# Optimization experiments

Hardware: AMD Instinct MI355X
Metric: run time of the kernel (lower is better)

The kernel has to match this reference:

```python
import jax, jax.numpy as jnp
import numpy as np

N, E = 50000, 800000
IN_DIM, HID, HEADS, OUT_DIM, NUM_CLASSES = 512, 128, 4, 64, 4


def setup_inputs() -> dict:
    key = jax.random.key(0)
    ks = jax.random.split(key, 18)
    g = lambda k, shape, s=0.05: (jax.random.normal(k, shape, dtype=jnp.float32) * s)
    x = jax.random.normal(ks[0], (N, IN_DIM), dtype=jnp.float32)
    edge_index = jax.random.randint(ks[1], (2, E), 0, N, dtype=jnp.int32)
    return {
        "x": x,
        "edge_index": edge_index,
        # GATConv layer 1 (heads=4, concat)
        "W1": g(ks[2], (IN_DIM, HEADS * HID)),
        "att_src1": g(ks[3], (HEADS, HID)),
        "att_dst1": g(ks[4], (HEADS, HID)),
        "b1": jnp.zeros((HEADS * HID,), jnp.float32),
        # GATConv layer 2 (heads=1, no concat)
        "W2": g(ks[5], (HEADS * HID, OUT_DIM)),
        "att_src2": g(ks[6], (1, OUT_DIM)),
        "att_dst2": g(ks[7], (1, OUT_DIM)),
        "b2": jnp.zeros((OUT_DIM,), jnp.float32),
        # intra_attention MLP: Linear(out,out) -> tanh -> Linear(out,1) -> softmax(dim=0)
        "Wa": g(ks[8], (OUT_DIM, OUT_DIM)),
        "ba": jnp.zeros((OUT_DIM,), jnp.float32),
        "wv": g(ks[9], (OUT_DIM, 1)),
        "bv": jnp.zeros((1,), jnp.float32),
        "class_attn": g(ks[10], (NUM_CLASSES, OUT_DIM), 0.3),
        # classifier
        "Wc": g(ks[11], (OUT_DIM, NUM_CLASSES)),
        "bc": jnp.zeros((NUM_CLASSES,), jnp.float32),
    }


def _gat_layer(x, src, dst, W, att_src, att_dst, heads, feat):
    """PyG GATConv: gather -> LeakyReLU score -> segment softmax -> scatter add."""
    n = x.shape[0]
    h = (x @ W).reshape(n, heads, feat)                     # [N,H,F]
    a_s = jnp.sum(h * att_src[None], axis=-1)               # [N,H]
    a_d = jnp.sum(h * att_dst[None], axis=-1)               # [N,H]
    e = jax.nn.leaky_relu(a_s[src] + a_d[dst], 0.2)         # [E,H]
    m = jax.ops.segment_max(e, dst, num_segments=n)         # per-dst max
    ex = jnp.exp(e - m[dst])
    s = jax.ops.segment_sum(ex, dst, num_segments=n)
    alpha = ex / (s[dst] + 1e-16)                           # [E,H]
    msg = h[src] * alpha[:, :, None]                        # [E,H,F]
    return jax.ops.segment_sum(msg, dst, num_segments=n)    # [N,H,F]


def reference(x, edge_index, W1, att_src1, att_dst1, b1, W2, att_src2, att_dst2,
              b2, Wa, ba, wv, bv, class_attn, Wc, bc):
    n = x.shape[0]
    loop = jnp.arange(n, dtype=edge_index.dtype)
    src = jnp.concatenate([edge_index[0], loop])            # add_self_loops=True
    dst = jnp.concatenate([edge_index[1], loop])

    h1 = _gat_layer(x, src, dst, W1, att_src1, att_dst1, HEADS, HID)
    h1 = h1.reshape(n, HEADS * HID) + b1                    # concat heads + bias
    h1 = jax.nn.elu(h1)

    h2 = _gat_layer(h1, src, dst, W2, att_src2, att_dst2, 1, OUT_DIM)
    h2 = h2.reshape(n, OUT_DIM) + b2                        # heads=1, concat=False

    # intra-sample attention, softmax over nodes (dim=0)
    scores = jnp.tanh(h2 @ Wa + ba) @ wv + bv               # [N,1]
    attw = jax.nn.softmax(scores, axis=0)
    xw = h2 * attw                                          # [N,OUT]

    xn = xw / jnp.maximum(jnp.linalg.norm(xw, axis=1, keepdims=True), 1e-12)
    cn = class_attn / jnp.maximum(
        jnp.linalg.norm(class_attn, axis=1, keepdims=True), 1e-12)
    inter_class_scores = xn @ cn.T                          # [N,C]

    out = xw @ Wc + bc                                      # [N,C]
    return out, xw, inter_class_scores
```

## Files before the change

### kernel.cpp

```cpp
#include <hip/hip_runtime.h>
#include <cstdint>
#include <cstddef>

typedef __attribute__((ext_vector_type(8))) short bf16x8;
typedef __attribute__((ext_vector_type(4))) float f32x4;
typedef __attribute__((ext_vector_type(8))) unsigned short u16x8;

__device__ __forceinline__ unsigned encf(float f) {
  unsigned u = __float_as_uint(f);
  return (u & 0x80000000u) ? ~u : (u | 0x80000000u);
}
__device__ __forceinline__ float decf(unsigned u) {
  return (u & 0x80000000u) ? __uint_as_float(u & 0x7FFFFFFFu) : __uint_as_float(~u);
}
__device__ __forceinline__ float lrelu02(float x) { return x > 0.f ? x : 0.2f * x; }
__device__ __forceinline__ unsigned short f2bf(float f) {
  unsigned u = __float_as_uint(f);
  unsigned r = u + 0x7FFFu + ((u >> 16) & 1u);
  return (unsigned short)(r >> 16);
}
__device__ __forceinline__ float bf2f(unsigned short b) {
  return __uint_as_float(((unsigned)b) << 16);
}

__device__ __forceinline__ void gll16(const void* g, void* l) {
  __builtin_amdgcn_global_load_lds(
      (const __attribute__((address_space(1))) void*)g,
      (__attribute__((address_space(3))) void*)l, 16, 0, 0);
}

__global__ void zero_int_k(int* __restrict__ p, int n) {
  int i = blockIdx.x * 256 + threadIdx.x;
  if (i < n) p[i] = 0;
}

__global__ void hist_k(const int* __restrict__ ei, int E, int N, int* __restrict__ counts) {
  int i = blockIdx.x * 256 + threadIdx.x;
  int Eall = E + N;
  if (i >= Eall) return;
  int dst = (i < E) ? ei[E + i] : (i - E);
  atomicAdd(&counts[dst], 1);
}

__global__ __launch_bounds__(256) void scan1_k(const int* __restrict__ counts,
                                               int* __restrict__ incl,
                                               int* __restrict__ bsum, int N) {
  int b = blockIdx.x, tid = threadIdx.x;
  int lane = tid & 63, wv = tid >> 6;
  int i = b * 256 + tid;
  int v = (i < N) ? counts[i] : 0;
#pragma unroll
  for (int o = 1; o < 64; o <<= 1) {
    int t = __shfl_up(v, o, 64);
    if (lane >= o) v += t;
  }
  __shared__ int wsum[4];
  if (lane == 63) wsum[wv] = v;
  __syncthreads();
  int base = 0;
  for (int wj = 0; wj < wv; wj++) base += wsum[wj];
  v += base;
  if (i < N) incl[i] = v;
  if (tid == 255) bsum[b] = v;
}

__global__ __launch_bounds__(256) void scan2_k(const int* __restrict__ bsum,
                                               int* __restrict__ pb, int nb) {
  int tid = threadIdx.x;
  int lane = tid & 63, wv = tid >> 6;
  int v = (tid < nb) ? bsum[tid] : 0;
  int orig = v;
#pragma unroll
  for (int o = 1; o < 64; o <<= 1) {
    int t = __shfl_up(v, o, 64);
    if (lane >= o) v += t;
  }
  __shared__ int wsum[4];
  if (lane == 63) wsum[wv] = v;
  __syncthreads();
  int base = 0;
  for (int wj = 0; wj < wv; wj++) base += wsum[wj];
  if (tid < nb) pb[tid] = v + base - orig;
}

__global__ void scan3_k(const int* __restrict__ incl, const int* __restrict__ pb,
                        int* __restrict__ offs, int* __restrict__ cursor, int N) {
  int i = blockIdx.x * 256 + threadIdx.x;
  if (i == 0) { offs[0] = 0; cursor[0] = 0; }
  if (i < N) {
    int v = incl[i] + pb[i >> 8];
    offs[i + 1] = v;
    if (i + 1 < N) cursor[i + 1] = v;
  }
}

__global__ void scatter_k(const int* __restrict__ ei, int E, int N,
                          int* __restrict__ cursor, int* __restrict__ ssrc) {
  int i = blockIdx.x * 256 + threadIdx.x;
  int Eall = E + N;
  if (i >= Eall) return;
  int src, dst;
  if (i < E) { src = ei[i]; dst = ei[E + i]; }
  else       { src = i - E; dst = i - E; }
  int pos = atomicAdd(&cursor[dst], 1);
  ssrc[pos] = src;
}

__global__ void conv_x_k(const float* __restrict__ x, unsigned short* __restrict__ xb,
                         int N, int Mpad) {
  int i = blockIdx.x * 256 + threadIdx.x;
  int total = Mpad * 64;
  if (i >= total) return;
  int row = i >> 6;
  u16x8 v;
  if (row < N) {
    const float4* src = (const float4*)(x + (size_t)i * 8);
    float4 a = src[0], b = src[1];
    v[0] = f2bf(a.x); v[1] = f2bf(a.y); v[2] = f2bf(a.z); v[3] = f2bf(a.w);
    v[4] = f2bf(b.x); v[5] = f2bf(b.y); v[6] = f2bf(b.z); v[7] = f2bf(b.w);
  } else {
    v = (u16x8)0;
  }
  *(u16x8*)(xb + (size_t)i * 8) = v;
}

__global__ void conv_wt_k(const float* __restrict__ W, unsigned short* __restrict__ Wt,
                          int K, int Nc) {
  int i = blockIdx.x * 256 + threadIdx.x;
  if (i >= K * Nc) return;
  int c = i / K, k = i - c * K;
  Wt[i] = f2bf(W[(size_t)k * Nc + c]);
}

__global__ __launch_bounds__(256, 2) void gemm1_k(const unsigned short* __restrict__ A,
                                                  const unsigned short* __restrict__ Bt,
                                                  unsigned short* __restrict__ C,
                                                  const float* __restrict__ att_s,
                                                  const float* __restrict__ att_d,
                                                  float* __restrict__ as_out,
                                                  float* __restrict__ ad_out,
                                                  int M, int K, int Nc) {
  __shared__ unsigned short As[128][64];
  __shared__ unsigned short Bs[256][64];
  __shared__ float s_ds[2][128];
  __shared__ float s_dd[2][128];
  const int tid = threadIdx.x;
  const int lane = tid & 63;
  const int w = tid >> 6;
  const int wr = w >> 1, wc = w & 1;
  const int l16 = lane & 15, lk = lane >> 4;
  const int row0 = blockIdx.x * 128, col0 = blockIdx.y * 256;

  f32x4 acc[4][8];
#pragma unroll
  for (int m = 0; m < 4; m++)
#pragma unroll
    for (int n = 0; n < 8; n++) acc[m][n] = (f32x4)0.f;

  const char* Abase = (const char*)A;
  const char* Bbase = (const char*)Bt;

  for (int k0 = 0; k0 < K; k0 += 64) {
#pragma unroll
    for (int i = 0; i < 4; i++) {
      int ca = i * 256 + tid;
      int r = ca >> 3, b = (ca & 7) * 16;
      gll16(Abase + ((size_t)(row0 + r) * K + k0) * 2 + b, (char*)&As[0][0] + ca * 16);
    }
#pragma unroll
    for (int i = 0; i < 8; i++) {
      int cb = i * 256 + tid;
      int c = cb >> 3, b = (cb & 7) * 16;
      gll16(Bbase + ((size_t)(col0 + c) * K + k0) * 2 + b, (char*)&Bs[0][0] + cb * 16);
    }
    __syncthreads();
#pragma unroll
    for (int ks = 0; ks < 2; ks++) {
      bf16x8 af[4], bfr[8];
#pragma unroll
      for (int m = 0; m < 4; m++)
        af[m] = *(const bf16x8*)&As[wr * 64 + m * 16 + l16][ks * 32 + lk * 8];
#pragma unroll
      for (int n = 0; n < 8; n++)
        bfr[n] = *(const bf16x8*)&Bs[wc * 128 + n * 16 + l16][ks * 32 + lk * 8];
#pragma unroll
      for (int m = 0; m < 4; m++)
#pragma unroll
        for (int n = 0; n < 8; n++)
          acc[m][n] = __builtin_amdgcn_mfma_f32_16x16x32_bf16(af[m], bfr[n], acc[m][n], 0, 0, 0);
    }
    __syncthreads();
  }
#pragma unroll
  for (int m = 0; m < 4; m++) {
    int row_b = row0 + wr * 64 + m * 16 + lk * 4;
#pragma unroll
    for (int r = 0; r < 4; r++) {
      int row = row_b + r;
      if (row < M) {
#pragma unroll
        for (int n = 0; n < 8; n++) {
          int col = col0 + wc * 128 + n * 16 + l16;
          C[(size_t)row * Nc + col] = f2bf(acc[m][n][r]);
        }
      }
    }
  }
  float as_c[8], ad_c[8];
#pragma unroll
  for (int n = 0; n < 8; n++) {
    int col = col0 + wc * 128 + n * 16 + l16;
    as_c[n] = att_s[col];
    ad_c[n] = att_d[col];
  }
#pragma unroll
  for (int m = 0; m < 4; m++) {
#pragma unroll
    for (int r = 0; r < 4; r++) {
      float ps = 0.f, pd = 0.f;
#pragma unroll
      for (int n = 0; n < 8; n++) {
        ps += acc[m][n][r] * as_c[n];
        pd += acc[m][n][r] * ad_c[n];
      }
#pragma unroll
      for (int o = 8; o; o >>= 1) { ps += __shfl_xor(ps, o); pd += __shfl_xor(pd, o); }
      if (l16 == 0) {
        int rr = wr * 64 + m * 16 + lk * 4 + r;
        s_ds[wc][rr] = ps;
        s_dd[wc][rr] = pd;
      }
    }
  }
  __syncthreads();
  if (tid < 128) {
    int row = row0 + tid;
    if (row < M) {
      int hb = 2 * blockIdx.y;
      as_out[(size_t)row * 4 + hb + 0] = s_ds[0][tid];
      as_out[(size_t)row * 4 + hb + 1] = s_ds[1][tid];
      ad_out[(size_t)row * 4 + hb + 0] = s_dd[0][tid];
      ad_out[(size_t)row * 4 + hb + 1] = s_dd[1][tid];
    }
  }
}

__global__ __launch_bounds__(256) void gemm2_k(const unsigned short* __restrict__ A,
                                               const unsigned short* __restrict__ Bt,
                                               unsigned short* __restrict__ C,
                                               const float* __restrict__ att_s,
                                               const float* __restrict__ att_d,
                                               float* __restrict__ as_out,
                                               float* __restrict__ ad_out,
                                               int M, int K, int Nc) {
  __shared__ unsigned short As[64][64];
  __shared__ unsigned short Bs[64][64];
  __shared__ float s_ds[2][64];
  __shared__ float s_dd[2][64];
  const int tid = threadIdx.x;
  const int lane = tid & 63;
  const int w = tid >> 6;
  const int wr = w >> 1, wc = w & 1;
  const int l16 = lane & 15, lk = lane >> 4;
  const int row0 = blockIdx.x * 64;

  f32x4 acc[2][2];
#pragma unroll
  for (int m = 0; m < 2; m++)
#pragma unroll
    for (int n = 0; n < 2; n++) acc[m][n] = (f32x4)0.f;

  const char* Abase = (const char*)A;
  const char* Bbase = (const char*)Bt;

  for (int k0 = 0; k0 < K; k0 += 64) {
#pragma unroll
    for (int i = 0; i < 2; i++) {
      int ca = i * 256 + tid;
      int r = ca >> 3, b = (ca & 7) * 16;
      gll16(Abase + ((size_t)(row0 + r) * K + k0) * 2 + b, (char*)&As[0][0] + ca * 16);
    }
#pragma unroll
    for (int i = 0; i < 2; i++) {
      int cb = i * 256 + tid;
      int c = cb >> 3, b = (cb & 7) * 16;
      gll16(Bbase + ((size_t)c * K + k0) * 2 + b, (char*)&Bs[0][0] + cb * 16);
    }
    __syncthreads();
#pragma unroll
    for (int ks = 0; ks < 2; ks++) {
      bf16x8 af[2], bfr[2];
#pragma unroll
      for (int m = 0; m < 2; m++)
        af[m] = *(const bf16x8*)&As[wr * 32 + m * 16 + l16][ks * 32 + lk * 8];
#pragma unroll
      for (int n = 0; n < 2; n++)
        bfr[n] = *(const bf16x8*)&Bs[wc * 32 + n * 16 + l16][ks * 32 + lk * 8];
#pragma unroll
      for (int m = 0; m < 2; m++)
#pragma unroll
        for (int n = 0; n < 2; n++)
          acc[m][n] = __builtin_amdgcn_mfma_f32_16x16x32_bf16(af[m], bfr[n], acc[m][n], 0, 0, 0);
    }
    __syncthreads();
  }
#pragma unroll
  for (int m = 0; m < 2; m++) {
    int row_b = row0 + wr * 32 + m * 16 + lk * 4;
#pragma unroll
    for (int r = 0; r < 4; r++) {
      int row = row_b + r;
      if (row < M) {
#pragma unroll
        for (int n = 0; n < 2; n++) {
          int col = wc * 32 + n * 16 + l16;
          C[(size_t)row * Nc + col] = f2bf(acc[m][n][r]);
        }
      }
    }
  }
  float as_c[2], ad_c[2];
#pragma unroll
  for (int n = 0; n < 2; n++) {
    int col = wc * 32 + n * 16 + l16;
    as_c[n] = att_s[col];
    ad_c[n] = att_d[col];
  }
#pragma unroll
  for (int m = 0; m < 2; m++) {
#pragma unroll
    for (int r = 0; r < 4; r++) {
      float ps = 0.f, pd = 0.f;
#pragma unroll
      for (int n = 0; n < 2; n++) {
        ps += acc[m][n][r] * as_c[n];
        pd += acc[m][n][r] * ad_c[n];
      }
#pragma unroll
      for (int o = 8; o; o >>= 1) { ps += __shfl_xor(ps, o); pd += __shfl_xor(pd, o); }
      if (l16 == 0) {
        int rr = wr * 32 + m * 16 + lk * 4 + r;
        s_ds[wc][rr] = ps;
        s_dd[wc][rr] = pd;
      }
    }
  }
  __syncthreads();
  if (tid < 64) {
    int row = row0 + tid;
    if (row < M) {
      as_out[row] = s_ds[0][tid] + s_ds[1][tid];
      ad_out[row] = s_dd[0][tid] + s_dd[1][tid];
    }
  }
}

__global__ __launch_bounds__(256) void gat_agg1_k(const unsigned short* __restrict__ hfeat,
                                                  const float* __restrict__ a_s,
                                                  const float* __restrict__ a_d,
                                                  const int* __restrict__ offs,
                                                  const int* __restrict__ ssrc,
                                                  const float* __restrict__ b1,
                                                  unsigned short* __restrict__ h1b, int N) {
  const int tid = threadIdx.x;
  const int lane = tid & 63, wave = tid >> 6;
  const int n = blockIdx.x * 4 + wave;
  if (n >= N) return;
  __shared__ int   s_src[4][64];
  __shared__ float s_ex[4][64][4];
  const int start = offs[n], end = offs[n + 1];
  const int hhl = lane >> 4;
  const float4 adv4 = *(const float4*)(a_d + (size_t)n * 4);
  const float4* as4 = (const float4*)a_s;

  float m0 = -1e30f, m1 = -1e30f, m2 = -1e30f, m3 = -1e30f;
  float S0 = 0.f, S1 = 0.f, S2 = 0.f, S3 = 0.f;
  float acc[8] = {0.f, 0.f, 0.f, 0.f, 0.f, 0.f, 0.f, 0.f};

  for (int base = start; base < end; base += 64) {
    const int cnt = min(64, end - base);
    float e0 = -1e30f, e1 = -1e30f, e2 = -1e30f, e3 = -1e30f;
    int s = 0;
    if (lane < cnt) {
      s = ssrc[base + lane];
      float4 av = as4[s];
      e0 = lrelu02(av.x + adv4.x);
      e1 = lrelu02(av.y + adv4.y);
      e2 = lrelu02(av.z + adv4.z);
      e3 = lrelu02(av.w + adv4.w);
    }
    float c0 = e0, c1 = e1, c2 = e2, c3 = e3;
#pragma unroll
    for (int o = 32; o; o >>= 1) {
      c0 = fmaxf(c0, __shfl_xor(c0, o));
      c1 = fmaxf(c1, __shfl_xor(c1, o));
      c2 = fmaxf(c2, __shfl_xor(c2, o));
      c3 = fmaxf(c3, __shfl_xor(c3, o));
    }
    float nm0 = fmaxf(m0, c0), nm1 = fmaxf(m1, c1);
    float nm2 = fmaxf(m2, c2), nm3 = fmaxf(m3, c3);
    float sc0 = __expf(m0 - nm0), sc1 = __expf(m1 - nm1);
    float sc2 = __expf(m2 - nm2), sc3 = __expf(m3 - nm3);
    m0 = nm0; m1 = nm1; m2 = nm2; m3 = nm3;
    float x0 = (lane < cnt) ? __expf(e0 - nm0) : 0.f;
    float x1 = (lane < cnt) ? __expf(e1 - nm1) : 0.f;
    float x2 = (lane < cnt) ? __expf(e2 - nm2) : 0.f;
    float x3 = (lane < cnt) ? __expf(e3 - nm3) : 0.f;
    s_src[wave][lane] = s;
    s_ex[wave][lane][0] = x0; s_ex[wave][lane][1] = x1;
    s_ex[wave][lane][2] = x2; s_ex[wave][lane][3] = x3;
#pragma unroll
    for (int o = 32; o; o >>= 1) {
      x0 += __shfl_xor(x0, o); x1 += __shfl_xor(x1, o);
      x2 += __shfl_xor(x2, o); x3 += __shfl_xor(x3, o);
    }
    S0 = S0 * sc0 + x0; S1 = S1 * sc1 + x1;
    S2 = S2 * sc2 + x2; S3 = S3 * sc3 + x3;
    float scl = (hhl == 0) ? sc0 : (hhl == 1) ? sc1 : (hhl == 2) ? sc2 : sc3;
#pragma unroll
    for (int q = 0; q < 8; q++) acc[q] *= scl;
#pragma unroll 4
    for (int j = 0; j < cnt; j++) {
      int sj = s_src[wave][j];
      float al = s_ex[wave][j][hhl];
      uint4 pk = *(const uint4*)(hfeat + ((size_t)sj << 9) + lane * 8);
      acc[0] += al * __uint_as_float(pk.x << 16);
      acc[1] += al * __uint_as_float(pk.x & 0xFFFF0000u);
      acc[2] += al * __uint_as_float(pk.y << 16);
      acc[3] += al * __uint_as_float(pk.y & 0xFFFF0000u);
      acc[4] += al * __uint_as_float(pk.z << 16);
      acc[5] += al * __uint_as_float(pk.z & 0xFFFF0000u);
      acc[6] += al * __uint_as_float(pk.w << 16);
      acc[7] += al * __uint_as_float(pk.w & 0xFFFF0000u);
    }
  }
  float inv = 1.f / (((hhl == 0) ? S0 : (hhl == 1) ? S1 : (hhl == 2) ? S2 : S3) + 1e-16f);
  const float4 b1a = *(const float4*)(b1 + lane * 8);
  const float4 b1b = *(const float4*)(b1 + lane * 8 + 4);
  float v[8];
  v[0] = acc[0] * inv + b1a.x; v[1] = acc[1] * inv + b1a.y;
  v[2] = acc[2] * inv + b1a.z; v[3] = acc[3] * inv + b1a.w;
  v[4] = acc[4] * inv + b1b.x; v[5] = acc[5] * inv + b1b.y;
  v[6] = acc[6] * inv + b1b.z; v[7] = acc[7] * inv + b1b.w;
  u16x8 outv;
#pragma unroll
  for (int q = 0; q < 8; q++) {
    float t = v[q] > 0.f ? v[q] : (__expf(v[q]) - 1.f);
    outv[q] = f2bf(t);
  }
  *(u16x8*)(h1b + ((size_t)n << 9) + lane * 8) = outv;
}

__global__ __launch_bounds__(256) void gat_agg2_k(const unsigned short* __restrict__ h2b,
                                                  const float* __restrict__ a_s,
                                                  const float* __restrict__ a_d,
                                                  const int* __restrict__ offs,
                                                  const int* __restrict__ ssrc,
                                                  const float* __restrict__ b2,
                                                  float* __restrict__ h2out, int N) {
  const int tid = threadIdx.x;
  const int lane = tid & 63, wave = tid >> 6;
  const int n = blockIdx.x * 4 + wave;
  if (n >= N) return;
  __shared__ int   s_src[4][64];
  __shared__ float s_ex[4][64];
  const int start = offs[n], end = offs[n + 1];
  const float ad = a_d[n];
  const int half = lane >> 5, l32 = lane & 31;

  float m = -1e30f, S = 0.f, acc0 = 0.f, acc1 = 0.f;
  for (int base = start; base < end; base += 64) {
    const int cnt = min(64, end - base);
    float e = -1e30f;
    int s = 0;
    if (lane < cnt) {
      s = ssrc[base + lane];
      e = lrelu02(a_s[s] + ad);
    }
    float c = e;
#pragma unroll
    for (int o = 32; o; o >>= 1) c = fmaxf(c, __shfl_xor(c, o));
    float nm = fmaxf(m, c);
    float sc = __expf(m - nm);
    m = nm;
    float x = (lane < cnt) ? __expf(e - nm) : 0.f;
    s_src[wave][lane] = s;
    s_ex[wave][lane] = x;
    float xs = x;
#pragma unroll
    for (int o = 32; o; o >>= 1) xs += __shfl_xor(xs, o);
    S = S * sc + xs;
    acc0 *= sc; acc1 *= sc;
#pragma unroll 4
    for (int j = half; j < cnt; j += 2) {
      int sj = s_src[wave][j];
      float al = s_ex[wave][j];
      unsigned pk = *(const unsigned*)(h2b + ((size_t)sj << 6) + l32 * 2);
      acc0 += al * __uint_as_float(pk << 16);
      acc1 += al * __uint_as_float(pk & 0xFFFF0000u);
    }
  }
  acc0 += __shfl_xor(acc0, 32);
  acc1 += __shfl_xor(acc1, 32);
  if (half == 0) {
    float inv = 1.f / (S + 1e-16f);
    float2 o;
    o.x = acc0 * inv + b2[l32 * 2];
    o.y = acc1 * inv + b2[l32 * 2 + 1];
    *(float2*)(h2out + ((size_t)n << 6) + l32 * 2) = o;
  }
}

__global__ __launch_bounds__(256) void score_k(const float* __restrict__ h2,
                                               const float* __restrict__ Wa,
                                               const float* __restrict__ ba,
                                               const float* __restrict__ wv,
                                               const float* __restrict__ bv,
                                               float* __restrict__ scores, int N) {
  int lane = threadIdx.x & 63, wave = threadIdx.x >> 6;
  int n = blockIdx.x * 4 + wave;
  if (n >= N) return;
  float hv = h2[(size_t)n * 64 + lane];
  float t = ba[lane];
  for (int k = 0; k < 64; k++) {
    float hk = __shfl(hv, k);
    t += hk * Wa[k * 64 + lane];
  }
  t = tanhf(t);
  float p = t * wv[lane];
#pragma unroll
  for (int o = 32; o; o >>= 1) p += __shfl_xor(p, o);
  if (lane == 0) scores[n] = p + bv[0];
}

__global__ void red_init_k(unsigned* __restrict__ red) {
  if (threadIdx.x == 0) { red[0] = 0x007FFFFFu; red[1] = 0u; }
}

__global__ void score_max_k(const float* __restrict__ scores, unsigned* __restrict__ red, int N) {
  int i = blockIdx.x * 256 + threadIdx.x;
  float m = (i < N) ? scores[i] : -1e30f;
#pragma unroll
  for (int o = 32; o; o >>= 1) m = fmaxf(m, __shfl_xor(m, o));
  if ((threadIdx.x & 63) == 0) atomicMax(&red[0], encf(m));
}

__global__ void score_sum_k(const float* __restrict__ scores, unsigned* __restrict__ red, int N) {
  float M = decf(red[0]);
  int i = blockIdx.x * 256 + threadIdx.x;
  float s = (i < N) ? __expf(scores[i] - M) : 0.f;
#pragma unroll
  for (int o = 32; o; o >>= 1) s += __shfl_xor(s, o);
  if ((threadIdx.x & 63) == 0) atomicAdd(reinterpret_cast<float*>(red) + 1, s);
}

__global__ void prep_cn_k(const float* __restrict__ ca, float* __restrict__ cn) {
  int lane = threadIdx.x & 63, c = threadIdx.x >> 6;
  float v = ca[c * 64 + lane];
  float p = v * v;
#pragma unroll
  for (int o = 32; o; o >>= 1) p += __shfl_xor(p, o);
  cn[c * 64 + lane] = v / fmaxf(sqrtf(p), 1e-12f);
}

__global__ __launch_bounds__(256) void finalize_k(const float* __restrict__ h2,
                                                  const float* __restrict__ scores,
                                                  const unsigned* __restrict__ red,
                                                  const float* __restrict__ cn,
                                                  const float* __restrict__ Wc,
                                                  const float* __restrict__ bc,
                                                  float* __restrict__ out, int N) {
  int lane = threadIdx.x & 63, wave = threadIdx.x >> 6;
  int n = blockIdx.x * 4 + wave;
  if (n >= N) return;
  float M = decf(red[0]);
  float S = __uint_as_float(red[1]);
  float attw = __expf(scores[n] - M) / S;
  float xw = h2[(size_t)n * 64 + lane] * attw;
  float p = xw * xw;
#pragma unroll
  for (int o = 32; o; o >>= 1) p += __shfl_xor(p, o);
  float xn = xw / fmaxf(sqrtf(p), 1e-12f);
  float i0 = xn * cn[lane],       i1 = xn * cn[64 + lane];
  float i2 = xn * cn[128 + lane], i3 = xn * cn[192 + lane];
  float o0 = xw * Wc[lane * 4 + 0], o1 = xw * Wc[lane * 4 + 1];
  float o2 = xw * Wc[lane * 4 + 2], o3 = xw * Wc[lane * 4 + 3];
#pragma unroll
  for (int o = 32; o; o >>= 1) {
    i0 += __shfl_xor(i0, o); i1 += __shfl_xor(i1, o);
    i2 += __shfl_xor(i2, o); i3 += __shfl_xor(i3, o);
    o0 += __shfl_xor(o0, o); o1 += __shfl_xor(o1, o);
    o2 += __shfl_xor(o2, o); o3 += __shfl_xor(o3, o);
  }
  float* outp   = out;
  float* xwp    = out + (size_t)N * 4;
  float* interp = out + (size_t)N * 68;
  xwp[(size_t)n * 64 + lane] = xw;
  if (lane == 0) {
    outp[n * 4 + 0] = o0 + bc[0]; outp[n * 4 + 1] = o1 + bc[1];
    outp[n * 4 + 2] = o2 + bc[2]; outp[n * 4 + 3] = o3 + bc[3];
    interp[n * 4 + 0] = i0; interp[n * 4 + 1] = i1;
    interp[n * 4 + 2] = i2; interp[n * 4 + 3] = i3;
  }
}

extern "C" void kernel_launch(void* const* d_in, const int* in_sizes, int n_in,
                              void* d_out, int out_size, void* d_ws, size_t ws_size,
                              hipStream_t stream) {
  const float* x        = (const float*)d_in[0];
  const int*   ei       = (const int*)d_in[1];
  const float* W1       = (const float*)d_in[2];
  const float* att_src1 = (const float*)d_in[3];
  const float* att_dst1 = (const float*)d_in[4];
  const float* b1       = (const float*)d_in[5];
  const float* W2       = (const float*)d_in[6];
  const float* att_src2 = (const float*)d_in[7];
  const float* att_dst2 = (const float*)d_in[8];
  const float* b2       = (const float*)d_in[9];
  const float* Wa       = (const float*)d_in[10];
  const float* ba       = (const float*)d_in[11];
  const float* wv       = (const float*)d_in[12];
  const float* bv       = (const float*)d_in[13];
  const float* class_attn = (const float*)d_in[14];
  const float* Wc       = (const float*)d_in[15];
  const float* bc       = (const float*)d_in[16];

  const int N = in_sizes[0] / 512;
  const int E = in_sizes[1] / 2;
  const int Eall = E + N;
  const int Mpad = ((N + 127) / 128) * 128;
  const int nb = (N + 255) / 256;

  char* w = (char*)d_ws;
  size_t off = 0;
  auto alloc = [&](size_t bytes) -> void* {
    off = (off + 255) & ~((size_t)255);
    void* p = w + off;
    off += bytes;
    return p;
  };
  unsigned short* xb  = (unsigned short*)alloc((size_t)Mpad * 512 * 2);
  unsigned short* h1b = xb;
  unsigned short* hb  = (unsigned short*)alloc((size_t)N * 512 * 2);
  unsigned short* h2b = (unsigned short*)alloc((size_t)N * 64 * 2);
  float* h2     = (float*)alloc((size_t)N * 64 * 4);
  unsigned short* W1t = (unsigned short*)alloc((size_t)512 * 512 * 2);
  unsigned short* W2t = (unsigned short*)alloc((size_t)64 * 512 * 2);
  float* as1    = (float*)alloc((size_t)N * 4 * 4);
  float* ad1    = (float*)alloc((size_t)N * 4 * 4);
  float* as2    = (float*)alloc((size_t)N * 4);
  float* ad2    = (float*)alloc((size_t)N * 4);
  int*   counts = (int*)alloc((size_t)N * 4);
  int*   incl   = (int*)alloc((size_t)N * 4);
  int*   bsum   = (int*)alloc(256 * 4);
  int*   pb     = (int*)alloc(256 * 4);
  int*   offs   = (int*)alloc((size_t)(N + 1) * 4);
  int*   cursor = (int*)alloc((size_t)N * 4);
  int*   ssrc   = (int*)alloc((size_t)Eall * 4);
  float* scores = (float*)alloc((size_t)N * 4);
  unsigned* red = (unsigned*)alloc(64);
  float* cn     = (float*)alloc(256 * 4);

  const int gN256  = (N + 255) / 256;
  const int gE256  = (Eall + 255) / 256;
  const int gNode4 = (N + 3) / 4;

  zero_int_k<<<gN256, 256, 0, stream>>>(counts, N);
  hist_k<<<gE256, 256, 0, stream>>>(ei, E, N, counts);
  scan1_k<<<nb, 256, 0, stream>>>(counts, incl, bsum, N);
  scan2_k<<<1, 256, 0, stream>>>(bsum, pb, nb);
  scan3_k<<<gN256, 256, 0, stream>>>(incl, pb, offs, cursor, N);
  scatter_k<<<gE256, 256, 0, stream>>>(ei, E, N, cursor, ssrc);

  conv_x_k<<<(Mpad * 64 + 255) / 256, 256, 0, stream>>>(x, xb, N, Mpad);
  conv_wt_k<<<(512 * 512 + 255) / 256, 256, 0, stream>>>(W1, W1t, 512, 512);
  conv_wt_k<<<(64 * 512 + 255) / 256, 256, 0, stream>>>(W2, W2t, 512, 64);

  gemm1_k<<<dim3(Mpad / 128, 2), 256, 0, stream>>>(
      xb, W1t, hb, att_src1, att_dst1, as1, ad1, N, 512, 512);
  gat_agg1_k<<<gNode4, 256, 0, stream>>>(hb, as1, ad1, offs, ssrc, b1, h1b, N);

  gemm2_k<<<dim3(Mpad / 64, 1), 256, 0, stream>>>(
      h1b, W2t, h2b, att_src2, att_dst2, as2, ad2, N, 512, 64);
  gat_agg2_k<<<gNode4, 256, 0, stream>>>(h2b, as2, ad2, offs, ssrc, b2, h2, N);

  score_k<<<gNode4, 256, 0, stream>>>(h2, Wa, ba, wv, bv, scores, N);
  red_init_k<<<1, 64, 0, stream>>>(red);
  score_max_k<<<gN256, 256, 0, stream>>>(scores, red, N);
  score_sum_k<<<gN256, 256, 0, stream>>>(scores, red, N);
  prep_cn_k<<<1, 256, 0, stream>>>(class_attn, cn);
  finalize_k<<<gNode4, 256, 0, stream>>>(h2, scores, red, cn, Wc, bc,
                                         (float*)d_out, N);
}
```

Before: 444.5 us.

## Fuse x conversion into GEMM1, fuse scoring into agg2, merge prep kernels

New measurement: 432.5 us. 2.7% less time.

```diff
diff --git a/kernel.cpp b/kernel.cpp
--- a/kernel.cpp
+++ b/kernel.cpp
@@ -27,11 +27,6 @@
   __builtin_amdgcn_global_load_lds(
       (const __attribute__((address_space(1))) void*)g,
       (__attribute__((address_space(3))) void*)l, 16, 0, 0);
-}
-
-__global__ void zero_int_k(int* __restrict__ p, int n) {
-  int i = blockIdx.x * 256 + threadIdx.x;
-  if (i < n) p[i] = 0;
 }
 
 __global__ void hist_k(const int* __restrict__ ei, int E, int N, int* __restrict__ counts) {
@@ -106,33 +101,34 @@
   ssrc[pos] = src;
 }
 
-__global__ void conv_x_k(const float* __restrict__ x, unsigned short* __restrict__ xb,
-                         int N, int Mpad) {
-  int i = blockIdx.x * 256 + threadIdx.x;
-  int total = Mpad * 64;
-  if (i >= total) return;
-  int row = i >> 6;
-  u16x8 v;
-  if (row < N) {
-    const float4* src = (const float4*)(x + (size_t)i * 8);
-    float4 a = src[0], b = src[1];
-    v[0] = f2bf(a.x); v[1] = f2bf(a.y); v[2] = f2bf(a.z); v[3] = f2bf(a.w);
-    v[4] = f2bf(b.x); v[5] = f2bf(b.y); v[6] = f2bf(b.z); v[7] = f2bf(b.w);
+__global__ void prep_k(const float* __restrict__ W1, unsigned short* __restrict__ W1t,
+                       const float* __restrict__ W2, unsigned short* __restrict__ W2t,
+                       const float* __restrict__ ca, float* __restrict__ cn,
+                       unsigned* __restrict__ red) {
+  const int b = blockIdx.x;
+  const int tid = threadIdx.x;
+  const int NB1 = 1024;
+  const int NB2 = 128;
+  if (b < NB1) {
+    int i = b * 256 + tid;
+    int c = i >> 9, k = i & 511;
+    W1t[i] = f2bf(W1[(size_t)k * 512 + c]);
+  } else if (b < NB1 + NB2) {
+    int i = (b - NB1) * 256 + tid;
+    int c = i >> 9, k = i & 511;
+    W2t[i] = f2bf(W2[(size_t)k * 64 + c]);
   } else {
-    v = (u16x8)0;
-  }
-  *(u16x8*)(xb + (size_t)i * 8) = v;
-}
-
-__global__ void conv_wt_k(const float* __restrict__ W, unsigned short* __restrict__ Wt,
-                          int K, int Nc) {
-  int i = blockIdx.x * 256 + threadIdx.x;
-  if (i >= K * Nc) return;
-  int c = i / K, k = i - c * K;
-  Wt[i] = f2bf(W[(size_t)k * Nc + c]);
-}
-
-__global__ __launch_bounds__(256, 2) void gemm1_k(const unsigned short* __restrict__ A,
+    int lane = tid & 63, c = tid >> 6;
+    float v = ca[c * 64 + lane];
+    float p = v * v;
+#pragma unroll
+    for (int o = 32; o; o >>= 1) p += __shfl_xor(p, o);
+    cn[c * 64 + lane] = v / fmaxf(sqrtf(p), 1e-12f);
+    if (tid == 0) { red[0] = 0x007FFFFFu; red[1] = 0u; }
+  }
+}
+
+__global__ __launch_bounds__(256, 2) void gemm1_k(const float* __restrict__ X,
                                                   const unsigned short* __restrict__ Bt,
                                                   unsigned short* __restrict__ C,
                                                   const float* __restrict__ att_s,
@@ -157,21 +153,28 @@
 #pragma unroll
     for (int n = 0; n < 8; n++) acc[m][n] = (f32x4)0.f;
 
-  const char* Abase = (const char*)A;
   const char* Bbase = (const char*)Bt;
 
   for (int k0 = 0; k0 < K; k0 += 64) {
-#pragma unroll
-    for (int i = 0; i < 4; i++) {
-      int ca = i * 256 + tid;
-      int r = ca >> 3, b = (ca & 7) * 16;
-      gll16(Abase + ((size_t)(row0 + r) * K + k0) * 2 + b, (char*)&As[0][0] + ca * 16);
-    }
 #pragma unroll
     for (int i = 0; i < 8; i++) {
       int cb = i * 256 + tid;
       int c = cb >> 3, b = (cb & 7) * 16;
       gll16(Bbase + ((size_t)(col0 + c) * K + k0) * 2 + b, (char*)&Bs[0][0] + cb * 16);
+    }
+#pragma unroll
+    for (int i = 0; i < 4; i++) {
+      int id = i * 256 + tid;
+      int r = id >> 3, c = (id & 7) * 8;
+      int row = row0 + r;
+      if (row >= M) row = M - 1;
+      const float* src = X + (size_t)row * K + k0 + c;
+      float4 a0 = *(const float4*)src;
+      float4 a1 = *(const float4*)(src + 4);
+      u16x8 pk;
+      pk[0] = f2bf(a0.x); pk[1] = f2bf(a0.y); pk[2] = f2bf(a0.z); pk[3] = f2bf(a0.w);
+      pk[4] = f2bf(a1.x); pk[5] = f2bf(a1.y); pk[6] = f2bf(a1.z); pk[7] = f2bf(a1.w);
+      *(u16x8*)&As[r][c] = pk;
     }
     __syncthreads();
 #pragma unroll
@@ -419,7 +422,7 @@
     float scl = (hhl == 0) ? sc0 : (hhl == 1) ? sc1 : (hhl == 2) ? sc2 : sc3;
 #pragma unroll
     for (int q = 0; q < 8; q++) acc[q] *= scl;
-#pragma unroll 4
+#pragma unroll 8
     for (int j = 0; j < cnt; j++) {
       int sj = s_src[wave][j];
       float al = s_ex[wave][j][hhl];
@@ -457,7 +460,12 @@
                                                   const int* __restrict__ offs,
                                                   const int* __restrict__ ssrc,
                                                   const float* __restrict__ b2,
-                                                  float* __restrict__ h2out, int N) {
+                                                  const float* __restrict__ Wa,
+                                                  const float* __restrict__ ba,
+                                                  const float* __restrict__ wv,
+                                                  const float* __restrict__ bv,
+                                                  float* __restrict__ h2out,
+                                                  float* __restrict__ scores, int N) {
   const int tid = threadIdx.x;
   const int lane = tid & 63, wave = tid >> 6;
   const int n = blockIdx.x * 4 + wave;
@@ -491,7 +499,7 @@
     for (int o = 32; o; o >>= 1) xs += __shfl_xor(xs, o);
     S = S * sc + xs;
     acc0 *= sc; acc1 *= sc;
-#pragma unroll 4
+#pragma unroll 8
     for (int j = half; j < cnt; j += 2) {
       int sj = s_src[wave][j];
       float al = s_ex[wave][j];
@@ -502,39 +510,26 @@
   }
   acc0 += __shfl_xor(acc0, 32);
   acc1 += __shfl_xor(acc1, 32);
+  float inv = 1.f / (S + 1e-16f);
+  float hx = acc0 * inv + b2[l32 * 2];
+  float hy = acc1 * inv + b2[l32 * 2 + 1];
   if (half == 0) {
-    float inv = 1.f / (S + 1e-16f);
     float2 o;
-    o.x = acc0 * inv + b2[l32 * 2];
-    o.y = acc1 * inv + b2[l32 * 2 + 1];
+    o.x = hx; o.y = hy;
     *(float2*)(h2out + ((size_t)n << 6) + l32 * 2) = o;
   }
-}
-
-__global__ __launch_bounds__(256) void score_k(const float* __restrict__ h2,
-                                               const float* __restrict__ Wa,
-                                               const float* __restrict__ ba,
-                                               const float* __restrict__ wv,
-                                               const float* __restrict__ bv,
-                                               float* __restrict__ scores, int N) {
-  int lane = threadIdx.x & 63, wave = threadIdx.x >> 6;
-  int n = blockIdx.x * 4 + wave;
-  if (n >= N) return;
-  float hv = h2[(size_t)n * 64 + lane];
   float t = ba[lane];
-  for (int k = 0; k < 64; k++) {
-    float hk = __shfl(hv, k);
-    t += hk * Wa[k * 64 + lane];
+#pragma unroll 8
+  for (int k = 0; k < 32; k++) {
+    float a = __shfl(hx, k);
+    float b = __shfl(hy, k);
+    t += a * Wa[(2 * k) * 64 + lane] + b * Wa[(2 * k + 1) * 64 + lane];
   }
   t = tanhf(t);
   float p = t * wv[lane];
 #pragma unroll
   for (int o = 32; o; o >>= 1) p += __shfl_xor(p, o);
   if (lane == 0) scores[n] = p + bv[0];
-}
-
-__global__ void red_init_k(unsigned* __restrict__ red) {
-  if (threadIdx.x == 0) { red[0] = 0x007FFFFFu; red[1] = 0u; }
 }
 
 __global__ void score_max_k(const float* __restrict__ scores, unsigned* __restrict__ red, int N) {
@@ -552,15 +547,6 @@
 #pragma unroll
   for (int o = 32; o; o >>= 1) s += __shfl_xor(s, o);
   if ((threadIdx.x & 63) == 0) atomicAdd(reinterpret_cast<float*>(red) + 1, s);
-}
-
-__global__ void prep_cn_k(const float* __restrict__ ca, float* __restrict__ cn) {
-  int lane = threadIdx.x & 63, c = threadIdx.x >> 6;
-  float v = ca[c * 64 + lane];
-  float p = v * v;
-#pragma unroll
-  for (int o = 32; o; o >>= 1) p += __shfl_xor(p, o);
-  cn[c * 64 + lane] = v / fmaxf(sqrtf(p), 1e-12f);
 }
 
 __global__ __launch_bounds__(256) void finalize_k(const float* __restrict__ h2,
@@ -639,8 +625,7 @@
     off += bytes;
     return p;
   };
-  unsigned short* xb  = (unsigned short*)alloc((size_t)Mpad * 512 * 2);
-  unsigned short* h1b = xb;
+  unsigned short* h1b = (unsigned short*)alloc((size_t)Mpad * 512 * 2);
   unsigned short* hb  = (unsigned short*)alloc((size_t)N * 512 * 2);
   unsigned short* h2b = (unsigned short*)alloc((size_t)N * 64 * 2);
   float* h2     = (float*)alloc((size_t)N * 64 * 4);
@@ -665,30 +650,26 @@
   const int gE256  = (Eall + 255) / 256;
   const int gNode4 = (N + 3) / 4;
 
-  zero_int_k<<<gN256, 256, 0, stream>>>(counts, N);
+  hipMemsetAsync(counts, 0, (size_t)N * 4, stream);
   hist_k<<<gE256, 256, 0, stream>>>(ei, E, N, counts);
   scan1_k<<<nb, 256, 0, stream>>>(counts, incl, bsum, N);
   scan2_k<<<1, 256, 0, stream>>>(bsum, pb, nb);
   scan3_k<<<gN256, 256, 0, stream>>>(incl, pb, offs, cursor, N);
   scatter_k<<<gE256, 256, 0, stream>>>(ei, E, N, cursor, ssrc);
 
-  conv_x_k<<<(Mpad * 64 + 255) / 256, 256, 0, stream>>>(x, xb, N, Mpad);
-  conv_wt_k<<<(512 * 512 + 255) / 256, 256, 0, stream>>>(W1, W1t, 512, 512);
-  conv_wt_k<<<(64 * 512 + 255) / 256, 256, 0, stream>>>(W2, W2t, 512, 64);
+  prep_k<<<1024 + 128 + 1, 256, 0, stream>>>(W1, W1t, W2, W2t, class_attn, cn, red);
 
   gemm1_k<<<dim3(Mpad / 128, 2), 256, 0, stream>>>(
-      xb, W1t, hb, att_src1, att_dst1, as1, ad1, N, 512, 512);
+      x, W1t, hb, att_src1, att_dst1, as1, ad1, N, 512, 512);
   gat_agg1_k<<<gNode4, 256, 0, stream>>>(hb, as1, ad1, offs, ssrc, b1, h1b, N);
 
   gemm2_k<<<dim3(Mpad / 64, 1), 256, 0, stream>>>(
       h1b, W2t, h2b, att_src2, att_dst2, as2, ad2, N, 512, 64);
-  gat_agg2_k<<<gNode4, 256, 0, stream>>>(h2b, as2, ad2, offs, ssrc, b2, h2, N);
-
-  score_k<<<gNode4, 256, 0, stream>>>(h2, Wa, ba, wv, bv, scores, N);
-  red_init_k<<<1, 64, 0, stream>>>(red);
+  gat_agg2_k<<<gNode4, 256, 0, stream>>>(h2b, as2, ad2, offs, ssrc, b2,
+                                         Wa, ba, wv, bv, h2, scores, N);
+
   score_max_k<<<gN256, 256, 0, stream>>>(scores, red, N);
   score_sum_k<<<gN256, 256, 0, stream>>>(scores, red, N);
-  prep_cn_k<<<1, 256, 0, stream>>>(class_attn, cn);
   finalize_k<<<gNode4, 256, 0, stream>>>(h2, scores, red, cn, Wc, bc,
                                          (float*)d_out, N);
 }
```
